# Kernel tuning notes

Hardware: AMD Instinct MI355X
Metric: run time of the kernel (lower is better)

Reference implementation:

```python
import jax, jax.numpy as jnp
import numpy as np

B, S, Q, D = 8, 2048, 2048, 1024  # additive path requires S == Q


def setup_inputs() -> dict:
    key = jax.random.key(0)
    ks = jax.random.split(key, 5)
    def glorot(k, shape):
        fan_in, fan_out = shape[0], shape[1]
        limit = np.sqrt(6.0 / (fan_in + fan_out)).astype(np.float32)
        return jax.random.uniform(k, shape, jnp.float32, -limit, limit)
    return {
        "source": jax.random.normal(ks[0], (B, S, D), jnp.float32),
        "query": jax.random.normal(ks[1], (B, Q, D), jnp.float32),
        "kernel": glorot(ks[2], (S, Q)),
        "wk_kernel": glorot(ks[3], (D, Q)),
        "wq_kernel": glorot(ks[4], (S, D)),
    }


def reference(source, query, kernel, wk_kernel, wq_kernel):
    # query permuted to (B, D, Q) as in call()
    q_t = jnp.transpose(query, (0, 2, 1))
    # additive similarity: tanh(Wk . Source + Wq . Query) . kernel
    f_att = (jnp.einsum("bsd,dq->bsq", source, wk_kernel)
             + jnp.einsum("sd,bdq->bsq", wq_kernel, q_t))  # (B, S, Q)
    sim = jnp.einsum("bsq,qt->bst", jnp.tanh(f_att), kernel)  # (B, S, Q)
    sm = jax.nn.softmax(sim, axis=-1)  # softmax over last axis (Keras default)
    # sm_t = permute(sm, (0,2,1)); result = batch_dot(sm_t, Source)
    return jnp.einsum("bsq,bsd->bqd", sm, source)  # (B, Q, D)
```

## Files before the change

kernel.cpp:

```cpp
#include <hip/hip_runtime.h>
#include <hip/hip_bf16.h>
#include <stdint.h>

typedef unsigned short u16;

#define B_ 8
#define S_ 2048
#define Q_ 2048
#define D_ 1024
#define T_ 2048

#define GRP 528

typedef __attribute__((ext_vector_type(8))) short short8;
typedef __attribute__((ext_vector_type(16))) float f32x16;

__device__ __forceinline__ u16 f2b(float f) {
  union { float f; uint32_t u; } x; x.f = f;
  uint32_t r = x.u + 0x7fffu + ((x.u >> 16) & 1u);
  return (u16)(r >> 16);
}
__device__ __forceinline__ float b2f(u16 h) {
  union { uint32_t u; float f; } x; x.u = ((uint32_t)h) << 16;
  return x.f;
}
__device__ __forceinline__ float tanh_fast(float x) {
  return 1.0f - 2.0f / (__expf(2.0f * x) + 1.0f);
}
__device__ __forceinline__ void async16(const void* g, void* l) {
  __builtin_amdgcn_global_load_lds(
      (const __attribute__((address_space(1))) void*)g,
      (__attribute__((address_space(3))) void*)l, 16, 0, 0);
}

__global__ void cast_f32_bf16_k(const float* __restrict__ in, u16* __restrict__ out, int n4) {
  int i = blockIdx.x * 256 + threadIdx.x;
  if (i >= n4) return;
  float4 v = ((const float4*)in)[i];
  uint32_t lo = (uint32_t)f2b(v.x) | ((uint32_t)f2b(v.y) << 16);
  uint32_t hi = (uint32_t)f2b(v.z) | ((uint32_t)f2b(v.w) << 16);
  ((uint2*)out)[i] = make_uint2(lo, hi);
}

__global__ void transpose_f32_bf16_k(const float* __restrict__ in, u16* __restrict__ out,
                                     int R, int C) {
  __shared__ float tile[32][33];
  int z = blockIdx.z;
  const float* pin = in + (size_t)z * R * C;
  u16* pout = out + (size_t)z * R * C;
  int c0 = blockIdx.x * 32, r0 = blockIdx.y * 32;
  int tx = threadIdx.x, ty = threadIdx.y;
#pragma unroll
  for (int k = 0; k < 32; k += 8)
    tile[ty + k][tx] = pin[(size_t)(r0 + ty + k) * C + (c0 + tx)];
  __syncthreads();
#pragma unroll
  for (int k = 0; k < 32; k += 8)
    pout[(size_t)(c0 + ty + k) * R + (r0 + tx)] = f2b(tile[tx][ty + k]);
}

__global__ void src_prep_k(const float* __restrict__ in, u16* __restrict__ outc,
                           u16* __restrict__ outT) {
  __shared__ float tile[32][33];
  int z = blockIdx.z;
  const float* pin = in + (size_t)z * S_ * D_;
  u16* pc = outc + (size_t)z * S_ * D_;
  u16* pt = outT + (size_t)z * S_ * D_;
  int c0 = blockIdx.x * 32, r0 = blockIdx.y * 32;
  int tx = threadIdx.x, ty = threadIdx.y;
#pragma unroll
  for (int k = 0; k < 32; k += 8) {
    float v = pin[(size_t)(r0 + ty + k) * D_ + (c0 + tx)];
    tile[ty + k][tx] = v;
    pc[(size_t)(r0 + ty + k) * D_ + (c0 + tx)] = f2b(v);
  }
  __syncthreads();
#pragma unroll
  for (int k = 0; k < 32; k += 8)
    pt[(size_t)(c0 + ty + k) * S_ + (r0 + tx)] = f2b(tile[tx][ty + k]);
}

__global__ void rowstat_k(const u16* __restrict__ in, float2* __restrict__ ml, int T) {
  int row = blockIdx.x, tid = threadIdx.x;
  size_t base = (size_t)row * T + (size_t)tid * 8;
  uint4 raw = *(const uint4*)(in + base);
  uint32_t w[4] = {raw.x, raw.y, raw.z, raw.w};
  float f[8];
#pragma unroll
  for (int i = 0; i < 4; ++i) {
    f[2 * i]     = b2f((u16)(w[i] & 0xffffu));
    f[2 * i + 1] = b2f((u16)(w[i] >> 16));
  }
  float m = f[0];
#pragma unroll
  for (int i = 1; i < 8; ++i) m = fmaxf(m, f[i]);
  for (int s = 32; s > 0; s >>= 1) m = fmaxf(m, __shfl_xor(m, s));
  __shared__ float red[8];
  int wave = tid >> 6, lane = tid & 63;
  if (lane == 0) red[wave] = m;
  __syncthreads();
  m = fmaxf(fmaxf(red[0], red[1]), fmaxf(red[2], red[3]));
  float s = 0.0f;
#pragma unroll
  for (int i = 0; i < 8; ++i) s += __expf(f[i] - m);
  for (int k = 32; k > 0; k >>= 1) s += __shfl_xor(s, k);
  if (lane == 0) red[4 + wave] = s;
  __syncthreads();
  if (tid == 0) {
    s = red[4] + red[5] + red[6] + red[7];
    ml[row] = make_float2(m, 1.0f / s);
  }
}

__global__ void sm_transpose_k(const u16* __restrict__ sim, const float2* __restrict__ ml,
                               u16* __restrict__ smT) {
  __shared__ u16 tile[32][33];
  int z = blockIdx.z;
  const u16* pin = sim + (size_t)z * S_ * T_;
  u16* pout = smT + (size_t)z * T_ * S_;
  int c0 = blockIdx.x * 32, r0 = blockIdx.y * 32;
  int tx = threadIdx.x, ty = threadIdx.y;
#pragma unroll
  for (int k = 0; k < 32; k += 8)
    tile[ty + k][tx] = pin[(size_t)(r0 + ty + k) * T_ + (c0 + tx)];
  float2 p = ml[(size_t)z * S_ + r0 + tx];
  __syncthreads();
#pragma unroll
  for (int k = 0; k < 32; k += 8)
    pout[(size_t)(c0 + ty + k) * S_ + (r0 + tx)] =
        f2b(__expf(b2f(tile[tx][ty + k]) - p.x) * p.y);
}

__global__ __launch_bounds__(256, 4) void gemm_bt_k(
    const u16* __restrict__ A1, long lda1, long bsA1,
    const u16* __restrict__ B1, long ldb1, long bsB1,
    const u16* __restrict__ A2, long lda2, long bsA2,
    const u16* __restrict__ B2, long ldb2, long bsB2,
    void* __restrict__ Cv, long ldc, long bsC,
    int K, int Srows, int nTerms, int mode) {
  __shared__ __align__(16) u16 lds_a[16 * GRP];
  __shared__ __align__(16) u16 lds_b[16 * GRP];
  const int m0 = blockIdx.y * 128;
  const int n0 = blockIdx.x * 128;
  const int b = m0 / Srows;
  const int s0 = m0 - b * Srows;
  const int tid = threadIdx.x;
  const int wave = tid >> 6, lane = tid & 63;
  const int wm = (wave >> 1) * 64, wn = (wave & 1) * 64;
  const int l31 = lane & 31, hi = lane >> 5;
  const int srow = lane >> 3, scol = (lane & 7) * 8;

  const int rA0 = wm + l31,      rA1 = wm + 32 + l31;
  const int rB0 = wn + l31,      rB1 = wn + 32 + l31;
  const int offA0 = (rA0 >> 3) * GRP + (rA0 & 7) * 64 + hi * 8;
  const int offA1 = (rA1 >> 3) * GRP + (rA1 & 7) * 64 + hi * 8;
  const int offB0 = (rB0 >> 3) * GRP + (rB0 & 7) * 64 + hi * 8;
  const int offB1 = (rB1 >> 3) * GRP + (rB1 & 7) * 64 + hi * 8;

  f32x16 acc[2][2];
#pragma unroll
  for (int i = 0; i < 2; ++i)
#pragma unroll
    for (int j = 0; j < 2; ++j)
#pragma unroll
      for (int r = 0; r < 16; ++r) acc[i][j][r] = 0.0f;

  const u16* pA[2];
  const u16* pB[2];
  long la[2], lb[2];
  pA[0] = A1 + (size_t)bsA1 * b + (size_t)s0 * lda1;
  pB[0] = B1 + (size_t)bsB1 * b + (size_t)n0 * ldb1;
  pA[1] = (nTerms > 1) ? (A2 + (size_t)bsA2 * b + (size_t)s0 * lda2) : pA[0];
  pB[1] = (nTerms > 1) ? (B2 + (size_t)bsB2 * b + (size_t)n0 * ldb2) : pB[0];
  la[0] = lda1; la[1] = lda2;
  lb[0] = ldb1; lb[1] = ldb2;

  for (int t = 0; t < nTerms; ++t) {
    const u16* gA = pA[t];
    const u16* gB = pB[t];
    const long sA = la[t], sB = lb[t];
    for (int kt = 0; kt < K; kt += 64) {
#pragma unroll
      for (int j = 0; j < 4; ++j) {
        const int ga = j * 4 + wave;
        async16(gA + (size_t)(ga * 8 + srow) * sA + (kt + scol), &lds_a[ga * GRP]);
        async16(gB + (size_t)(ga * 8 + srow) * sB + (kt + scol), &lds_b[ga * GRP]);
      }
      __syncthreads();
#pragma unroll
      for (int kk = 0; kk < 4; ++kk) {
        short8 a0 = *(const short8*)&lds_a[offA0 + kk * 16];
        short8 a1 = *(const short8*)&lds_a[offA1 + kk * 16];
        short8 b0 = *(const short8*)&lds_b[offB0 + kk * 16];
        short8 b1 = *(const short8*)&lds_b[offB1 + kk * 16];
        acc[0][0] = __builtin_amdgcn_mfma_f32_32x32x16_bf16(a0, b0, acc[0][0], 0, 0, 0);
        acc[0][1] = __builtin_amdgcn_mfma_f32_32x32x16_bf16(a0, b1, acc[0][1], 0, 0, 0);
        acc[1][0] = __builtin_amdgcn_mfma_f32_32x32x16_bf16(a1, b0, acc[1][0], 0, 0, 0);
        acc[1][1] = __builtin_amdgcn_mfma_f32_32x32x16_bf16(a1, b1, acc[1][1], 0, 0, 0);
      }
      __syncthreads();
    }
  }

  const size_t cbase = (size_t)bsC * b + (size_t)s0 * ldc + n0;
  if (mode == 2) {
    float* C = (float*)Cv + cbase;
#pragma unroll
    for (int mi = 0; mi < 2; ++mi)
#pragma unroll
      for (int ni = 0; ni < 2; ++ni) {
        const int col = wn + ni * 32 + l31;
#pragma unroll
        for (int r = 0; r < 16; ++r) {
          const int row = wm + mi * 32 + (r & 3) + 8 * (r >> 2) + 4 * hi;
          C[(size_t)row * ldc + col] = acc[mi][ni][r];
        }
      }
  } else {
    u16* C = (u16*)Cv + cbase;
#pragma unroll
    for (int mi = 0; mi < 2; ++mi)
#pragma unroll
      for (int ni = 0; ni < 2; ++ni) {
        const int col = wn + ni * 32 + l31;
#pragma unroll
        for (int r = 0; r < 16; ++r) {
          const int row = wm + mi * 32 + (r & 3) + 8 * (r >> 2) + 4 * hi;
          float v = acc[mi][ni][r];
          if (mode == 0) v = tanh_fast(v);
          C[(size_t)row * ldc + col] = f2b(v);
        }
      }
  }
}

extern "C" void kernel_launch(void* const* d_in, const int* in_sizes, int n_in,
                              void* d_out, int out_size, void* d_ws, size_t ws_size,
                              hipStream_t stream) {
  const float* src = (const float*)d_in[0];
  const float* qry = (const float*)d_in[1];
  const float* ker = (const float*)d_in[2];
  const float* wk  = (const float*)d_in[3];
  const float* wq  = (const float*)d_in[4];
  float* out = (float*)d_out;
  u16* ws = (u16*)d_ws;

  u16* srcb  = ws;
  u16* qryb  = srcb  + (size_t)B_ * S_ * D_;
  u16* wqb   = qryb  + (size_t)B_ * Q_ * D_;
  u16* wkT   = wqb   + (size_t)S_ * D_;
  u16* kerT  = wkT   + (size_t)D_ * Q_;
  u16* srcT  = kerT  + (size_t)Q_ * T_;
  u16* tanhT = srcT  + (size_t)B_ * D_ * S_;
  u16* simb  = tanhT + (size_t)B_ * S_ * Q_;
  float2* ml = (float2*)wkT;

  dim3 tb(32, 8);

  cast_f32_bf16_k<<<(B_ * Q_ * D_) / 1024, 256, 0, stream>>>(qry, qryb, (B_ * Q_ * D_) / 4);
  cast_f32_bf16_k<<<(S_ * D_) / 1024, 256, 0, stream>>>(wq, wqb, (S_ * D_) / 4);
  transpose_f32_bf16_k<<<dim3(Q_ / 32, D_ / 32, 1), tb, 0, stream>>>(wk, wkT, D_, Q_);
  transpose_f32_bf16_k<<<dim3(T_ / 32, Q_ / 32, 1), tb, 0, stream>>>(ker, kerT, Q_, T_);
  src_prep_k<<<dim3(D_ / 32, S_ / 32, B_), tb, 0, stream>>>(src, srcb, srcT);

  gemm_bt_k<<<dim3(Q_ / 128, (B_ * S_) / 128), 256, 0, stream>>>(
      srcb, D_, (long)S_ * D_,
      wkT, D_, 0,
      wqb, D_, 0,
      qryb, D_, (long)Q_ * D_,
      tanhT, Q_, (long)S_ * Q_,
      D_, S_, 2, 0);

  gemm_bt_k<<<dim3(T_ / 128, (B_ * S_) / 128), 256, 0, stream>>>(
      tanhT, Q_, (long)S_ * Q_,
      kerT, Q_, 0,
      nullptr, 0, 0, nullptr, 0, 0,
      simb, T_, (long)S_ * T_,
      Q_, S_, 1, 1);

  rowstat_k<<<B_ * S_, 256, 0, stream>>>(simb, ml, T_);

  sm_transpose_k<<<dim3(T_ / 32, S_ / 32, B_), tb, 0, stream>>>(simb, ml, tanhT);

  gemm_bt_k<<<dim3(D_ / 128, (B_ * T_) / 128), 256, 0, stream>>>(
      tanhT, S_, (long)T_ * S_,
      srcT, S_, (long)D_ * S_,
      nullptr, 0, 0, nullptr, 0, 0,
      out, D_, (long)T_ * D_,
      S_, T_, 1, 2);
}
```

Before: 647.0 us.

## Fuse softmax exp and row sums into sim GEMM epilogue with transposed output

The sim GEMM epilogue now applies exp directly, atomically accumulates per-row sums, and writes the exponentiated tile transposed through LDS. This removes the separate rowstat and softmax-transpose kernels. Normalization moves onto source: srcT is scaled by 1/l per row before the final GEMM. The transpose prep kernels are also reworked into 64x64 tiles with vectorized loads and stores. Dropping the max subtraction relies on tanh-bounded logits, since |tanh| ≤ 1 bounds each logit by the L1 norm of a kernel column. Overflow of exp is therefore unlikely, but the change adds atomics and extra bf16 rounding on the scaled source.

Result: faster. 632.8 us (-2.2%).

```diff
diff --git a/kernel.cpp b/kernel.cpp
--- a/kernel.cpp
+++ b/kernel.cpp
@@ -42,93 +42,89 @@
   ((uint2*)out)[i] = make_uint2(lo, hi);
 }
 
-__global__ void transpose_f32_bf16_k(const float* __restrict__ in, u16* __restrict__ out,
+__global__ void transpose_f32_bf16_v(const float* __restrict__ in, u16* __restrict__ out,
                                      int R, int C) {
-  __shared__ float tile[32][33];
+  __shared__ u16 t[64 * 72];
   int z = blockIdx.z;
   const float* pin = in + (size_t)z * R * C;
   u16* pout = out + (size_t)z * R * C;
-  int c0 = blockIdx.x * 32, r0 = blockIdx.y * 32;
-  int tx = threadIdx.x, ty = threadIdx.y;
-#pragma unroll
-  for (int k = 0; k < 32; k += 8)
-    tile[ty + k][tx] = pin[(size_t)(r0 + ty + k) * C + (c0 + tx)];
+  int c0 = blockIdx.x * 64, r0 = blockIdx.y * 64;
+  int tid = threadIdx.x;
+  int rr = tid >> 4, c4 = (tid & 15) * 4;
+#pragma unroll
+  for (int p = 0; p < 4; ++p) {
+    int r = p * 16 + rr;
+    float4 v = *(const float4*)&pin[(size_t)(r0 + r) * C + c0 + c4];
+    t[(c4 + 0) * 72 + r] = f2b(v.x);
+    t[(c4 + 1) * 72 + r] = f2b(v.y);
+    t[(c4 + 2) * 72 + r] = f2b(v.z);
+    t[(c4 + 3) * 72 + r] = f2b(v.w);
+  }
   __syncthreads();
-#pragma unroll
-  for (int k = 0; k < 32; k += 8)
-    pout[(size_t)(c0 + ty + k) * R + (r0 + tx)] = f2b(tile[tx][ty + k]);
-}
-
-__global__ void src_prep_k(const float* __restrict__ in, u16* __restrict__ outc,
+  int ct = tid >> 3, r8 = (tid & 7) * 8;
+#pragma unroll
+  for (int p = 0; p < 2; ++p) {
+    int c = p * 32 + ct;
+    uint2 lo = *(const uint2*)&t[c * 72 + r8];
+    uint2 hi = *(const uint2*)&t[c * 72 + r8 + 4];
+    *(uint4*)&pout[(size_t)(c0 + c) * R + r0 + r8] = make_uint4(lo.x, lo.y, hi.x, hi.y);
+  }
+}
+
+__global__ void src_prep_v(const float* __restrict__ in, u16* __restrict__ outc,
                            u16* __restrict__ outT) {
-  __shared__ float tile[32][33];
+  __shared__ u16 t[64 * 72];
   int z = blockIdx.z;
   const float* pin = in + (size_t)z * S_ * D_;
   u16* pc = outc + (size_t)z * S_ * D_;
   u16* pt = outT + (size_t)z * S_ * D_;
-  int c0 = blockIdx.x * 32, r0 = blockIdx.y * 32;
-  int tx = threadIdx.x, ty = threadIdx.y;
-#pragma unroll
-  for (int k = 0; k < 32; k += 8) {
-    float v = pin[(size_t)(r0 + ty + k) * D_ + (c0 + tx)];
-    tile[ty + k][tx] = v;
-    pc[(size_t)(r0 + ty + k) * D_ + (c0 + tx)] = f2b(v);
+  int c0 = blockIdx.x * 64, r0 = blockIdx.y * 64;
+  int tid = threadIdx.x;
+  int rr = tid >> 4, c4 = (tid & 15) * 4;
+#pragma unroll
+  for (int p = 0; p < 4; ++p) {
+    int r = p * 16 + rr;
+    float4 v = *(const float4*)&pin[(size_t)(r0 + r) * D_ + c0 + c4];
+    u16 b0 = f2b(v.x), b1 = f2b(v.y), b2 = f2b(v.z), b3 = f2b(v.w);
+    uint2 pk;
+    pk.x = (uint32_t)b0 | ((uint32_t)b1 << 16);
+    pk.y = (uint32_t)b2 | ((uint32_t)b3 << 16);
+    *(uint2*)&pc[(size_t)(r0 + r) * D_ + c0 + c4] = pk;
+    t[(c4 + 0) * 72 + r] = b0;
+    t[(c4 + 1) * 72 + r] = b1;
+    t[(c4 + 2) * 72 + r] = b2;
+    t[(c4 + 3) * 72 + r] = b3;
   }
   __syncthreads();
-#pragma unroll
-  for (int k = 0; k < 32; k += 8)
-    pt[(size_t)(c0 + ty + k) * S_ + (r0 + tx)] = f2b(tile[tx][ty + k]);
-}
-
-__global__ void rowstat_k(const u16* __restrict__ in, float2* __restrict__ ml, int T) {
-  int row = blockIdx.x, tid = threadIdx.x;
-  size_t base = (size_t)row * T + (size_t)tid * 8;
-  uint4 raw = *(const uint4*)(in + base);
+  int ct = tid >> 3, r8 = (tid & 7) * 8;
+#pragma unroll
+  for (int p = 0; p < 2; ++p) {
+    int c = p * 32 + ct;
+    uint2 lo = *(const uint2*)&t[c * 72 + r8];
+    uint2 hi = *(const uint2*)&t[c * 72 + r8 + 4];
+    *(uint4*)&pt[(size_t)(c0 + c) * S_ + r0 + r8] = make_uint4(lo.x, lo.y, hi.x, hi.y);
+  }
+}
+
+__global__ void scale_srcT_k(u16* __restrict__ srcT, const float* __restrict__ l) {
+  size_t i = (size_t)blockIdx.x * 256 + threadIdx.x;
+  size_t e0 = i * 8;
+  int s8 = (int)(e0 & (S_ - 1));
+  int bb = (int)(e0 / ((size_t)D_ * S_));
+  const float* lp = l + (size_t)bb * S_ + s8;
+  float4 l0 = *(const float4*)lp;
+  float4 l1 = *(const float4*)(lp + 4);
+  uint4 raw = *(uint4*)&srcT[e0];
   uint32_t w[4] = {raw.x, raw.y, raw.z, raw.w};
-  float f[8];
-#pragma unroll
-  for (int i = 0; i < 4; ++i) {
-    f[2 * i]     = b2f((u16)(w[i] & 0xffffu));
-    f[2 * i + 1] = b2f((u16)(w[i] >> 16));
-  }
-  float m = f[0];
-#pragma unroll
-  for (int i = 1; i < 8; ++i) m = fmaxf(m, f[i]);
-  for (int s = 32; s > 0; s >>= 1) m = fmaxf(m, __shfl_xor(m, s));
-  __shared__ float red[8];
-  int wave = tid >> 6, lane = tid & 63;
-  if (lane == 0) red[wave] = m;
-  __syncthreads();
-  m = fmaxf(fmaxf(red[0], red[1]), fmaxf(red[2], red[3]));
-  float s = 0.0f;
-#pragma unroll
-  for (int i = 0; i < 8; ++i) s += __expf(f[i] - m);
-  for (int k = 32; k > 0; k >>= 1) s += __shfl_xor(s, k);
-  if (lane == 0) red[4 + wave] = s;
-  __syncthreads();
-  if (tid == 0) {
-    s = red[4] + red[5] + red[6] + red[7];
-    ml[row] = make_float2(m, 1.0f / s);
-  }
-}
-
-__global__ void sm_transpose_k(const u16* __restrict__ sim, const float2* __restrict__ ml,
-                               u16* __restrict__ smT) {
-  __shared__ u16 tile[32][33];
-  int z = blockIdx.z;
-  const u16* pin = sim + (size_t)z * S_ * T_;
-  u16* pout = smT + (size_t)z * T_ * S_;
-  int c0 = blockIdx.x * 32, r0 = blockIdx.y * 32;
-  int tx = threadIdx.x, ty = threadIdx.y;
-#pragma unroll
-  for (int k = 0; k < 32; k += 8)
-    tile[ty + k][tx] = pin[(size_t)(r0 + ty + k) * T_ + (c0 + tx)];
-  float2 p = ml[(size_t)z * S_ + r0 + tx];
-  __syncthreads();
-#pragma unroll
-  for (int k = 0; k < 32; k += 8)
-    pout[(size_t)(c0 + ty + k) * S_ + (r0 + tx)] =
-        f2b(__expf(b2f(tile[tx][ty + k]) - p.x) * p.y);
+  float li[8] = {l0.x, l0.y, l0.z, l0.w, l1.x, l1.y, l1.z, l1.w};
+  uint32_t o[4];
+#pragma unroll
+  for (int k = 0; k < 4; ++k) {
+    float a = b2f((u16)(w[k] & 0xffffu)) / li[2 * k];
+    float b = b2f((u16)(w[k] >> 16)) / li[2 * k + 1];
+    o[k] = (uint32_t)f2b(a) | ((uint32_t)f2b(b) << 16);
+  }
+  *(uint4*)&srcT[e0] = make_uint4(o[0], o[1], o[2], o[3]);
 }
 
 __global__ __launch_bounds__(256, 4) void gemm_bt_k(
@@ -137,9 +133,10 @@
     const u16* __restrict__ A2, long lda2, long bsA2,
     const u16* __restrict__ B2, long ldb2, long bsB2,
     void* __restrict__ Cv, long ldc, long bsC,
-    int K, int Srows, int nTerms, int mode) {
-  __shared__ __align__(16) u16 lds_a[16 * GRP];
-  __shared__ __align__(16) u16 lds_b[16 * GRP];
+    int K, int Srows, int nTerms, int mode, float* __restrict__ lsum) {
+  __shared__ __align__(16) u16 lds_all[32 * GRP];
+  u16* lds_a = lds_all;
+  u16* lds_b = lds_all + 16 * GRP;
   const int m0 = blockIdx.y * 128;
   const int n0 = blockIdx.x * 128;
   const int b = m0 / Srows;
@@ -200,6 +197,59 @@
       }
       __syncthreads();
     }
+  }
+
+  if (mode == 3) {
+#pragma unroll
+    for (int mi = 0; mi < 2; ++mi)
+#pragma unroll
+      for (int ni = 0; ni < 2; ++ni)
+#pragma unroll
+        for (int r = 0; r < 16; ++r)
+          acc[mi][ni][r] = __expf(acc[mi][ni][r]);
+    float* lrow = lsum + (size_t)b * Srows + s0;
+#pragma unroll
+    for (int mi = 0; mi < 2; ++mi)
+#pragma unroll
+      for (int r = 0; r < 16; ++r) {
+        float pv = acc[mi][0][r] + acc[mi][1][r];
+        pv += __shfl_xor(pv, 1);
+        pv += __shfl_xor(pv, 2);
+        pv += __shfl_xor(pv, 4);
+        pv += __shfl_xor(pv, 8);
+        pv += __shfl_xor(pv, 16);
+        const int row = wm + mi * 32 + (r & 3) + 8 * (r >> 2) + 4 * hi;
+        if (l31 == 0) atomicAdd(&lrow[row], pv);
+      }
+#pragma unroll
+    for (int mi = 0; mi < 2; ++mi)
+#pragma unroll
+      for (int ni = 0; ni < 2; ++ni) {
+        const int col = wn + ni * 32 + l31;
+#pragma unroll
+        for (int g = 0; g < 4; ++g) {
+          const int rowb = wm + mi * 32 + g * 8 + 4 * hi;
+          u16 p0 = f2b(acc[mi][ni][g * 4 + 0]);
+          u16 p1 = f2b(acc[mi][ni][g * 4 + 1]);
+          u16 p2 = f2b(acc[mi][ni][g * 4 + 2]);
+          u16 p3 = f2b(acc[mi][ni][g * 4 + 3]);
+          uint2 pk;
+          pk.x = (uint32_t)p0 | ((uint32_t)p1 << 16);
+          pk.y = (uint32_t)p2 | ((uint32_t)p3 << 16);
+          *(uint2*)&lds_all[col * 132 + rowb] = pk;
+        }
+      }
+    __syncthreads();
+    u16* gP = (u16*)Cv + (size_t)bsC * b + (size_t)n0 * ldc + s0;
+    const int tl = tid >> 4, s8 = (tid & 15) * 8;
+#pragma unroll
+    for (int p = 0; p < 8; ++p) {
+      const int tt = p * 16 + tl;
+      uint2 lo = *(const uint2*)&lds_all[tt * 132 + s8];
+      uint2 hi2 = *(const uint2*)&lds_all[tt * 132 + s8 + 4];
+      *(uint4*)&gP[(size_t)tt * ldc + s8] = make_uint4(lo.x, lo.y, hi2.x, hi2.y);
+    }
+    return;
   }
 
   const size_t cbase = (size_t)bsC * b + (size_t)s0 * ldc + n0;
@@ -252,16 +302,17 @@
   u16* kerT  = wkT   + (size_t)D_ * Q_;
   u16* srcT  = kerT  + (size_t)Q_ * T_;
   u16* tanhT = srcT  + (size_t)B_ * D_ * S_;
-  u16* simb  = tanhT + (size_t)B_ * S_ * Q_;
-  float2* ml = (float2*)wkT;
-
-  dim3 tb(32, 8);
+  u16* PT    = tanhT + (size_t)B_ * S_ * Q_;
+  float* l   = (float*)(PT + (size_t)B_ * T_ * S_);
+
+  dim3 tb(256);
 
   cast_f32_bf16_k<<<(B_ * Q_ * D_) / 1024, 256, 0, stream>>>(qry, qryb, (B_ * Q_ * D_) / 4);
   cast_f32_bf16_k<<<(S_ * D_) / 1024, 256, 0, stream>>>(wq, wqb, (S_ * D_) / 4);
-  transpose_f32_bf16_k<<<dim3(Q_ / 32, D_ / 32, 1), tb, 0, stream>>>(wk, wkT, D_, Q_);
-  transpose_f32_bf16_k<<<dim3(T_ / 32, Q_ / 32, 1), tb, 0, stream>>>(ker, kerT, Q_, T_);
-  src_prep_k<<<dim3(D_ / 32, S_ / 32, B_), tb, 0, stream>>>(src, srcb, srcT);
+  transpose_f32_bf16_v<<<dim3(Q_ / 64, D_ / 64, 1), tb, 0, stream>>>(wk, wkT, D_, Q_);
+  transpose_f32_bf16_v<<<dim3(T_ / 64, Q_ / 64, 1), tb, 0, stream>>>(ker, kerT, Q_, T_);
+  src_prep_v<<<dim3(D_ / 64, S_ / 64, B_), tb, 0, stream>>>(src, srcb, srcT);
+  hipMemsetAsync(l, 0, (size_t)B_ * S_ * sizeof(float), stream);
 
   gemm_bt_k<<<dim3(Q_ / 128, (B_ * S_) / 128), 256, 0, stream>>>(
       srcb, D_, (long)S_ * D_,
@@ -269,23 +320,21 @@
       wqb, D_, 0,
       qryb, D_, (long)Q_ * D_,
       tanhT, Q_, (long)S_ * Q_,
-      D_, S_, 2, 0);
+      D_, S_, 2, 0, nullptr);
 
   gemm_bt_k<<<dim3(T_ / 128, (B_ * S_) / 128), 256, 0, stream>>>(
       tanhT, Q_, (long)S_ * Q_,
       kerT, Q_, 0,
       nullptr, 0, 0, nullptr, 0, 0,
-      simb, T_, (long)S_ * T_,
-      Q_, S_, 1, 1);
-
-  rowstat_k<<<B_ * S_, 256, 0, stream>>>(simb, ml, T_);
-
-  sm_transpose_k<<<dim3(T_ / 32, S_ / 32, B_), tb, 0, stream>>>(simb, ml, tanhT);
+      PT, S_, (long)T_ * S_,
+      Q_, S_, 1, 3, l);
+
+  scale_srcT_k<<<(B_ * D_ * S_) / (256 * 8), 256, 0, stream>>>(srcT, l);
 
   gemm_bt_k<<<dim3(D_ / 128, (B_ * T_) / 128), 256, 0, stream>>>(
-      tanhT, S_, (long)T_ * S_,
+      PT, S_, (long)T_ * S_,
       srcT, S_, (long)D_ * S_,
       nullptr, 0, 0, nullptr, 0, 0,
       out, D_, (long)T_ * D_,
-      S_, T_, 1, 2);
-}
+      S_, T_, 1, 2, nullptr);
+}
```
